# Optimization experiments

Measured on AMD Instinct MI355X. Metric: run time of the kernel, lower is better.

Reference implementation:

```python
import jax, jax.numpy as jnp
import numpy as np

B, IN, H = 4096, 1024, 1024


def setup_inputs() -> dict:
    key = jax.random.key(0)
    ks = jax.random.split(key, 20)
    s_in = 1.0 / np.sqrt(IN)
    s_h = 1.0 / np.sqrt(H)
    def lin(kw, kb, fan_in, scale):
        W = jax.random.uniform(kw, (H, fan_in), jnp.float32, -scale, scale)
        b = jax.random.uniform(kb, (H,), jnp.float32, -scale, scale)
        return W, b
    Wxf, bxf = lin(ks[0], ks[1], IN, s_in)
    Whf, bhf = lin(ks[2], ks[3], H, s_h)
    Wxi, bxi = lin(ks[4], ks[5], IN, s_in)
    Whi, bhi = lin(ks[6], ks[7], H, s_h)
    Wxo, bxo = lin(ks[8], ks[9], IN, s_in)
    Who, bho = lin(ks[10], ks[11], H, s_h)
    Wxc, bxc = lin(ks[12], ks[13], IN, s_in)
    Whc, bhc = lin(ks[14], ks[15], H, s_h)
    x = jax.random.normal(ks[16], (B, IN), jnp.float32)
    c = jax.random.normal(ks[17], (B, H), jnp.float32)
    h = jax.random.normal(ks[18], (B, H), jnp.float32)
    return dict(x=x, c=c, h=h,
                Wxf=Wxf, bxf=bxf, Whf=Whf, bhf=bhf,
                Wxi=Wxi, bxi=bxi, Whi=Whi, bhi=bhi,
                Wxo=Wxo, bxo=bxo, Who=Who, bho=bho,
                Wxc=Wxc, bxc=bxc, Whc=Whc, bhc=bhc)


def reference(x, c, h,
              Wxf, bxf, Whf, bhf,
              Wxi, bxi, Whi, bhi,
              Wxo, bxo, Who, bho,
              Wxc, bxc, Whc, bhc):
    # Fuse the 8 small GEMMs into two batched GEMMs: x @ Wx^T and h @ Wh^T
    # with gate outputs concatenated along the hidden dim [f, i, o, c~].
    Wx = jnp.concatenate([Wxf, Wxi, Wxo, Wxc], axis=0)   # [4H, IN]
    Wh = jnp.concatenate([Whf, Whi, Who, Whc], axis=0)   # [4H, H]
    bx = jnp.concatenate([bxf, bxi, bxo, bxc], axis=0)   # [4H]
    bh = jnp.concatenate([bhf, bhi, bho, bhc], axis=0)   # [4H]
    gates = x @ Wx.T + h @ Wh.T + (bx + bh)              # [B, 4H]
    hs = Wxf.shape[0]
    f = jax.nn.sigmoid(gates[:, 0 * hs:1 * hs])
    i = jax.nn.sigmoid(gates[:, 1 * hs:2 * hs])
    o = jax.nn.sigmoid(gates[:, 2 * hs:3 * hs])
    ctil = jnp.tanh(gates[:, 3 * hs:4 * hs])
    ct = f * c + ctil * i
    ht = jnp.tanh(ct) * o
    return (ct, ht)
```

## Files before the change

kernel.cpp:

```cpp
#include <hip/hip_runtime.h>
#include <hip/hip_bf16.h>
#include <stdint.h>

typedef __hip_bfloat16 bf16;
typedef __attribute__((ext_vector_type(8))) short short8;
typedef __attribute__((ext_vector_type(4))) float floatx4;

#define AS1(p) ((const __attribute__((address_space(1))) void*)(p))
#define AS3(p) ((__attribute__((address_space(3))) void*)(p))

#define M_DIM 4096
#define H_DIM 1024
#define MEG   (1u << 20)
#define LDS_BUF 24576

__device__ __forceinline__ unsigned short f2bf(float f) {
    uint32_t u = __float_as_uint(f);
    uint32_t r = (u + 0x7FFFu + ((u >> 16) & 1u)) >> 16;
    return (unsigned short)r;
}

__device__ __forceinline__ float fast_sigmoid(float v) {
    return 1.0f / (1.0f + __expf(-v));
}
__device__ __forceinline__ float fast_tanh(float v) {
    return 2.0f / (1.0f + __expf(-2.0f * v)) - 1.0f;
}

__global__ __launch_bounds__(256)
void convert_to_bf16(const float* __restrict__ x, const float* __restrict__ h,
                     const float* Wxf, const float* Wxi, const float* Wxo, const float* Wxc,
                     const float* Whf, const float* Whi, const float* Who, const float* Whc,
                     unsigned short* __restrict__ ws)
{
    const uint32_t idx0 = blockIdx.x * 2048u + threadIdx.x * 8u;
    const uint32_t t = blockIdx.x >> 9;
    const float* src;
    uint32_t off;
    if (t < 4u)      { src = x; off = idx0; }
    else if (t < 8u) { src = h; off = idx0 - (4u << 20); }
    else {
        const uint32_t g = t - 8u;
        src = (g == 0) ? Wxf : (g == 1) ? Wxi : (g == 2) ? Wxo : (g == 3) ? Wxc
            : (g == 4) ? Whf : (g == 5) ? Whi : (g == 6) ? Who : Whc;
        off = idx0 & (MEG - 1u);
    }
    const float4 v0 = *(const float4*)(src + off);
    const float4 v1 = *(const float4*)(src + off + 4);
    short8 pk;
    pk[0] = (short)f2bf(v0.x); pk[1] = (short)f2bf(v0.y);
    pk[2] = (short)f2bf(v0.z); pk[3] = (short)f2bf(v0.w);
    pk[4] = (short)f2bf(v1.x); pk[5] = (short)f2bf(v1.y);
    pk[6] = (short)f2bf(v1.z); pk[7] = (short)f2bf(v1.w);
    *(short8*)(ws + idx0) = pk;
}

__global__ __launch_bounds__(256, 2)
void lstm_fused_kernel(const unsigned short* __restrict__ ws,
                       const float* __restrict__ c,
                       const float* __restrict__ bxf, const float* __restrict__ bhf,
                       const float* __restrict__ bxi, const float* __restrict__ bhi,
                       const float* __restrict__ bxo, const float* __restrict__ bho,
                       const float* __restrict__ bxc, const float* __restrict__ bhc,
                       float* __restrict__ out)
{
    __shared__ __align__(16) char lds[3 * LDS_BUF];

    const int tid  = threadIdx.x;
    const int w    = tid >> 6;
    const int lane = tid & 63;

    const int bid = blockIdx.x;
    const int mx  = bid >> 4;
    const int ny  = ((bid & 7) << 1) | ((bid >> 3) & 1);
    const int bm0 = mx * 128;
    const int bn0 = ny * 64;

    const uint32_t cg = (((uint32_t)lane & 3u) ^ (((uint32_t)lane >> 3) & 3u)) * 8u;
    const unsigned short* srcP0[6];
    const unsigned short* srcP1[6];
    uint32_t goff[6];
    uint32_t loff[6];
#pragma unroll
    for (int i = 0; i < 6; ++i) {
        const int ch = w * 6 + i;
        if (ch < 8) {
            const int row = bm0 + ch * 16 + (lane >> 2);
            srcP0[i] = ws;
            srcP1[i] = ws + (4u << 20);
            goff[i] = (uint32_t)row * 1024u + cg;
            loff[i] = (uint32_t)ch * 1024u;
        } else {
            const int b = ch - 8;
            const int g = b >> 2;
            const int n = bn0 + (b & 3) * 16 + (lane >> 2);
            srcP0[i] = ws + (8u << 20)  + (uint32_t)g * MEG;
            srcP1[i] = ws + (12u << 20) + (uint32_t)g * MEG;
            goff[i] = (uint32_t)n * 1024u + cg;
            loff[i] = 8192u + (uint32_t)b * 1024u;
        }
    }

    const int wrow  = (w & 1) * 64;
    const int wcol  = (w >> 1) * 32;
    const int lrc   = lane & 15;
    const int lquad = lane >> 4;

    const uint32_t kslot = (((uint32_t)lquad ^ (((uint32_t)lrc >> 1) & 3u))) * 8u;

    uint32_t aoff[4];
#pragma unroll
    for (int mt = 0; mt < 4; ++mt)
        aoff[mt] = (uint32_t)((wrow + mt * 16 + lrc) * 32) + kslot;
    uint32_t boff[4][2];
#pragma unroll
    for (int g = 0; g < 4; ++g)
#pragma unroll
        for (int nt = 0; nt < 2; ++nt)
            boff[g][nt] = (uint32_t)(g * 2048 + (wcol + nt * 16 + lrc) * 32) + kslot;

    floatx4 acc[4][4][2];
#pragma unroll
    for (int g = 0; g < 4; ++g)
#pragma unroll
        for (int mt = 0; mt < 4; ++mt)
#pragma unroll
            for (int nt = 0; nt < 2; ++nt)
                acc[g][mt][nt] = (floatx4){0.f, 0.f, 0.f, 0.f};

    auto issue_loads = [&](int kt, uint32_t stage) {
        const int phase = kt >> 5;
        const uint32_t k0 = (uint32_t)(kt & 31) * 32u;
        const uint32_t bb = stage * LDS_BUF;
#pragma unroll
        for (int i = 0; i < 6; ++i) {
            const unsigned short* src = phase ? srcP1[i] : srcP0[i];
            __builtin_amdgcn_global_load_lds(AS1(src + goff[i] + k0),
                                             AS3(lds + bb + loff[i]), 16, 0, 0);
        }
    };
    auto compute = [&](uint32_t stage) {
        const char* base = lds + stage * LDS_BUF;
        const bf16* lA = (const bf16*)base;
        const bf16* lB = (const bf16*)(base + 8192);
        short8 afr[4];
#pragma unroll
        for (int mt = 0; mt < 4; ++mt)
            afr[mt] = *(const short8*)(lA + aoff[mt]);
#pragma unroll
        for (int g = 0; g < 4; ++g) {
#pragma unroll
            for (int nt = 0; nt < 2; ++nt) {
                const short8 bfr = *(const short8*)(lB + boff[g][nt]);
#pragma unroll
                for (int mt = 0; mt < 4; ++mt)
                    acc[g][mt][nt] = __builtin_amdgcn_mfma_f32_16x16x32_bf16(
                        afr[mt], bfr, acc[g][mt][nt], 0, 0, 0);
            }
        }
    };

    issue_loads(0, 0);
    issue_loads(1, 1);

    uint32_t s_comp = 0;
    uint32_t s_load = 2;
    for (int kt = 0; kt < 62; ++kt) {
        asm volatile("s_waitcnt vmcnt(6)\ns_barrier" ::: "memory");
        issue_loads(kt + 2, s_load);
        compute(s_comp);
        s_comp = (s_comp == 2) ? 0 : s_comp + 1;
        s_load = (s_load == 2) ? 0 : s_load + 1;
    }
    asm volatile("s_waitcnt vmcnt(6)\ns_barrier" ::: "memory");
    compute(s_comp);
    s_comp = (s_comp == 2) ? 0 : s_comp + 1;
    asm volatile("s_waitcnt vmcnt(0)\ns_barrier" ::: "memory");
    compute(s_comp);

    float* out_ct = out;
    float* out_ht = out + (size_t)M_DIM * H_DIM;
#pragma unroll
    for (int nt = 0; nt < 2; ++nt) {
        const int col = bn0 + wcol + nt * 16 + lrc;
        const float bf_ = bxf[col] + bhf[col];
        const float bi_ = bxi[col] + bhi[col];
        const float bo_ = bxo[col] + bho[col];
        const float bc_ = bxc[col] + bhc[col];
#pragma unroll
        for (int mt = 0; mt < 4; ++mt) {
#pragma unroll
            for (int r = 0; r < 4; ++r) {
                const int row = bm0 + wrow + mt * 16 + lquad * 4 + r;
                const float gf = acc[0][mt][nt][r] + bf_;
                const float gi = acc[1][mt][nt][r] + bi_;
                const float go = acc[2][mt][nt][r] + bo_;
                const float gc = acc[3][mt][nt][r] + bc_;
                const float f    = fast_sigmoid(gf);
                const float ii   = fast_sigmoid(gi);
                const float o    = fast_sigmoid(go);
                const float ctil = fast_tanh(gc);
                const float cv   = c[(size_t)row * H_DIM + col];
                const float ctn  = f * cv + ctil * ii;
                const float htn  = fast_tanh(ctn) * o;
                out_ct[(size_t)row * H_DIM + col] = ctn;
                out_ht[(size_t)row * H_DIM + col] = htn;
            }
        }
    }
}

extern "C" void kernel_launch(void* const* d_in, const int* in_sizes, int n_in,
                              void* d_out, int out_size, void* d_ws, size_t ws_size,
                              hipStream_t stream) {
    (void)in_sizes; (void)n_in; (void)out_size; (void)ws_size;
    const float* x   = (const float*)d_in[0];
    const float* c   = (const float*)d_in[1];
    const float* h   = (const float*)d_in[2];
    const float* Wxf = (const float*)d_in[3];  const float* bxf = (const float*)d_in[4];
    const float* Whf = (const float*)d_in[5];  const float* bhf = (const float*)d_in[6];
    const float* Wxi = (const float*)d_in[7];  const float* bxi = (const float*)d_in[8];
    const float* Whi = (const float*)d_in[9];  const float* bhi = (const float*)d_in[10];
    const float* Wxo = (const float*)d_in[11]; const float* bxo = (const float*)d_in[12];
    const float* Who = (const float*)d_in[13]; const float* bho = (const float*)d_in[14];
    const float* Wxc = (const float*)d_in[15]; const float* bxc = (const float*)d_in[16];
    const float* Whc = (const float*)d_in[17]; const float* bhc = (const float*)d_in[18];
    float* out = (float*)d_out;
    unsigned short* ws = (unsigned short*)d_ws;

    convert_to_bf16<<<8192, 256, 0, stream>>>(x, h,
        Wxf, Wxi, Wxo, Wxc, Whf, Whi, Who, Whc, ws);

    lstm_fused_kernel<<<512, 256, 0, stream>>>(ws, c,
        bxf, bhf, bxi, bhi, bxo, bho, bxc, bhc, out);
}
```

Before: 224.3 us.

## Split block work across eight waves instead of four

Doubles the workgroup to 512 threads (8 waves), so each wave covers a 64x16 output slice per gate instead of 64x32. That halves the accumulator registers per wave, and each wave issues 3 global-to-LDS loads per stage instead of 6, with the wait counts adjusted to match. The goal is more waves in flight to hide memory and MFMA latency. The cost is more barrier participants and less register-level reuse of A fragments, since each A fragment now feeds fewer MFMAs per LDS read.

After: 217.0 us. 3.3% less time.

```diff
diff --git a/kernel.cpp b/kernel.cpp
--- a/kernel.cpp
+++ b/kernel.cpp
@@ -55,7 +55,7 @@
     *(short8*)(ws + idx0) = pk;
 }
 
-__global__ __launch_bounds__(256, 2)
+__global__ __launch_bounds__(512, 4)
 void lstm_fused_kernel(const unsigned short* __restrict__ ws,
                        const float* __restrict__ c,
                        const float* __restrict__ bxf, const float* __restrict__ bhf,
@@ -77,13 +77,13 @@
     const int bn0 = ny * 64;
 
     const uint32_t cg = (((uint32_t)lane & 3u) ^ (((uint32_t)lane >> 3) & 3u)) * 8u;
-    const unsigned short* srcP0[6];
-    const unsigned short* srcP1[6];
-    uint32_t goff[6];
-    uint32_t loff[6];
-#pragma unroll
-    for (int i = 0; i < 6; ++i) {
-        const int ch = w * 6 + i;
+    const unsigned short* srcP0[3];
+    const unsigned short* srcP1[3];
+    uint32_t goff[3];
+    uint32_t loff[3];
+#pragma unroll
+    for (int i = 0; i < 3; ++i) {
+        const int ch = w * 3 + i;
         if (ch < 8) {
             const int row = bm0 + ch * 16 + (lane >> 2);
             srcP0[i] = ws;
@@ -102,7 +102,7 @@
     }
 
     const int wrow  = (w & 1) * 64;
-    const int wcol  = (w >> 1) * 32;
+    const int wcol  = (w >> 1) * 16;
     const int lrc   = lane & 15;
     const int lquad = lane >> 4;
 
@@ -112,28 +112,24 @@
 #pragma unroll
     for (int mt = 0; mt < 4; ++mt)
         aoff[mt] = (uint32_t)((wrow + mt * 16 + lrc) * 32) + kslot;
-    uint32_t boff[4][2];
+    uint32_t boff[4];
 #pragma unroll
     for (int g = 0; g < 4; ++g)
-#pragma unroll
-        for (int nt = 0; nt < 2; ++nt)
-            boff[g][nt] = (uint32_t)(g * 2048 + (wcol + nt * 16 + lrc) * 32) + kslot;
-
-    floatx4 acc[4][4][2];
+        boff[g] = (uint32_t)(g * 2048 + (wcol + lrc) * 32) + kslot;
+
+    floatx4 acc[4][4];
 #pragma unroll
     for (int g = 0; g < 4; ++g)
 #pragma unroll
         for (int mt = 0; mt < 4; ++mt)
-#pragma unroll
-            for (int nt = 0; nt < 2; ++nt)
-                acc[g][mt][nt] = (floatx4){0.f, 0.f, 0.f, 0.f};
+            acc[g][mt] = (floatx4){0.f, 0.f, 0.f, 0.f};
 
     auto issue_loads = [&](int kt, uint32_t stage) {
         const int phase = kt >> 5;
         const uint32_t k0 = (uint32_t)(kt & 31) * 32u;
         const uint32_t bb = stage * LDS_BUF;
 #pragma unroll
-        for (int i = 0; i < 6; ++i) {
+        for (int i = 0; i < 3; ++i) {
             const unsigned short* src = phase ? srcP1[i] : srcP0[i];
             __builtin_amdgcn_global_load_lds(AS1(src + goff[i] + k0),
                                              AS3(lds + bb + loff[i]), 16, 0, 0);
@@ -149,14 +145,11 @@
             afr[mt] = *(const short8*)(lA + aoff[mt]);
 #pragma unroll
         for (int g = 0; g < 4; ++g) {
-#pragma unroll
-            for (int nt = 0; nt < 2; ++nt) {
-                const short8 bfr = *(const short8*)(lB + boff[g][nt]);
-#pragma unroll
-                for (int mt = 0; mt < 4; ++mt)
-                    acc[g][mt][nt] = __builtin_amdgcn_mfma_f32_16x16x32_bf16(
-                        afr[mt], bfr, acc[g][mt][nt], 0, 0, 0);
-            }
+            const short8 bfr = *(const short8*)(lB + boff[g]);
+#pragma unroll
+            for (int mt = 0; mt < 4; ++mt)
+                acc[g][mt] = __builtin_amdgcn_mfma_f32_16x16x32_bf16(
+                    afr[mt], bfr, acc[g][mt], 0, 0, 0);
         }
     };
 
@@ -166,13 +159,13 @@
     uint32_t s_comp = 0;
     uint32_t s_load = 2;
     for (int kt = 0; kt < 62; ++kt) {
-        asm volatile("s_waitcnt vmcnt(6)\ns_barrier" ::: "memory");
+        asm volatile("s_waitcnt vmcnt(3)\ns_barrier" ::: "memory");
         issue_loads(kt + 2, s_load);
         compute(s_comp);
         s_comp = (s_comp == 2) ? 0 : s_comp + 1;
         s_load = (s_load == 2) ? 0 : s_load + 1;
     }
-    asm volatile("s_waitcnt vmcnt(6)\ns_barrier" ::: "memory");
+    asm volatile("s_waitcnt vmcnt(3)\ns_barrier" ::: "memory");
     compute(s_comp);
     s_comp = (s_comp == 2) ? 0 : s_comp + 1;
     asm volatile("s_waitcnt vmcnt(0)\ns_barrier" ::: "memory");
@@ -180,9 +173,8 @@
 
     float* out_ct = out;
     float* out_ht = out + (size_t)M_DIM * H_DIM;
-#pragma unroll
-    for (int nt = 0; nt < 2; ++nt) {
-        const int col = bn0 + wcol + nt * 16 + lrc;
+    {
+        const int col = bn0 + wcol + lrc;
         const float bf_ = bxf[col] + bhf[col];
         const float bi_ = bxi[col] + bhi[col];
         const float bo_ = bxo[col] + bho[col];
@@ -192,10 +184,10 @@
 #pragma unroll
             for (int r = 0; r < 4; ++r) {
                 const int row = bm0 + wrow + mt * 16 + lquad * 4 + r;
-                const float gf = acc[0][mt][nt][r] + bf_;
-                const float gi = acc[1][mt][nt][r] + bi_;
-                const float go = acc[2][mt][nt][r] + bo_;
-                const float gc = acc[3][mt][nt][r] + bc_;
+                const float gf = acc[0][mt][r] + bf_;
+                const float gi = acc[1][mt][r] + bi_;
+                const float go = acc[2][mt][r] + bo_;
+                const float gc = acc[3][mt][r] + bc_;
                 const float f    = fast_sigmoid(gf);
                 const float ii   = fast_sigmoid(gi);
                 const float o    = fast_sigmoid(go);
@@ -231,6 +223,6 @@
     convert_to_bf16<<<8192, 256, 0, stream>>>(x, h,
         Wxf, Wxi, Wxo, Wxc, Whf, Whi, Who, Whc, ws);
 
-    lstm_fused_kernel<<<512, 256, 0, stream>>>(ws, c,
+    lstm_fused_kernel<<<512, 512, 0, stream>>>(ws, c,
         bxf, bhf, bxi, bhi, bxo, bho, bxc, bhc, out);
 }
```
